# Performance work log

Hardware: AMD Instinct MI355X
Metric: run time of the kernel (lower is better)

The kernel has to match this reference:

```python
import jax, jax.numpy as jnp
import numpy as np

N, E = 8192, 16384
IN_C, HID = 64, 64
ALPHA, BETA = -1.5, -0.5
DENSITY = 0.004


def setup_inputs() -> dict:
    key = jax.random.key(0)
    k_x, k_b, k_w0, k_w1 = jax.random.split(key, 4)
    x_0 = jax.random.normal(k_x, (N, IN_C), dtype=jnp.float32)
    # sparse binary incidence matrix (stored dense, as in the original module)
    B1 = (jax.random.uniform(k_b, (N, E)) < DENSITY).astype(jnp.float32)
    # guarantee every node and every hyperedge has at least one incidence
    B1 = B1.at[jnp.arange(N), jnp.arange(N) % E].set(1.0)
    B1 = B1.at[jnp.arange(E) % N, jnp.arange(E)].set(1.0)
    W0 = jax.random.normal(k_w0, (IN_C, HID), dtype=jnp.float32) * (1.0 / np.sqrt(IN_C))
    W1 = jax.random.normal(k_w1, (HID, HID), dtype=jnp.float32) * (1.0 / np.sqrt(HID))
    bias_0_to_1 = jnp.zeros((1, HID), dtype=jnp.float32)
    bias_1_to_0 = jnp.zeros((1, HID), dtype=jnp.float32)
    return {"x_0": x_0, "incidence_1": B1, "W0": W0, "W1": W1,
            "bias_0_to_1": bias_0_to_1, "bias_1_to_0": bias_1_to_0}


def _normalize_incidence(B1):
    # vectorized equivalent of the O(N*E) python double loop
    mask = (B1 != 0).astype(B1.dtype)                  # [N,E]
    edge_sum = B1.sum(axis=0)                          # [E] hyperedge sizes
    node_sum = B1.sum(axis=1)                          # [N] node degrees
    edge_norm = edge_sum ** ALPHA                      # [E]
    node_norm = node_sum ** BETA                       # [N]
    # edge_factor[i] = 1 / sum_j mask[i,j]*edge_norm[j]  (row mat-vec)
    row_fac = 1.0 / (mask @ edge_norm)                 # [N]
    # node_factor[j] = 1 / sum_i mask[i,j]*node_norm[i]  (col mat-vec)
    col_fac = 1.0 / (mask.T @ node_norm)               # [E]
    return B1 * (row_fac * node_norm)[:, None] * (edge_norm * col_fac)[None, :]


def reference(x_0, incidence_1, W0, W1, bias_0_to_1, bias_1_to_0):
    B = _normalize_incidence(incidence_1)              # [N,E]
    # conv 0 -> 1: x_1 = B^T @ (x_0 @ W0) + b
    x_1 = B.T @ (x_0 @ W0) + bias_0_to_1               # [E,HID]
    # conv 1 -> 0: x_0' = B @ (x_1 @ W1) + b
    x_0_out = B @ (x_1 @ W1) + bias_1_to_0             # [N,HID]
    return jax.nn.relu(x_0_out), jax.nn.relu(x_1)
```

## Files before the change

kernel.cpp:

```cpp
#include <hip/hip_runtime.h>
#include <hip/hip_bf16.h>
#include <stdint.h>

#define NN 8192
#define NE 16384
#define HIDW 64
#define RCAP 128
#define CCAP 96

#define OFF_ROWCNT   0u
#define OFF_COLCNT   (OFF_ROWCNT + NN*4u)
#define MEMSET_BYTES (OFF_COLCNT + NE*4u)
#define OFF_ENORM    MEMSET_BYTES
#define OFF_NNORM    (OFF_ENORM + NE*4u)
#define OFF_RSCALE   (OFF_NNORM + NN*4u)
#define OFF_CSCALE   (OFF_RSCALE + NN*4u)
#define OFF_CSR      (OFF_CSCALE + NE*4u)
#define OFF_CSC      (OFF_CSR + NN*RCAP*4u)
#define OFF_Y0       (OFF_CSC + (size_t)NE*CCAP*4u)
#define OFF_X1PRE    (OFF_Y0 + NN*HIDW*4u)
#define OFF_Z1       (OFF_X1PRE + (size_t)NE*HIDW*4u)

__global__ __launch_bounds__(256) void k_scan(const float* __restrict__ B1,
        uint32_t* __restrict__ row_cnt, uint32_t* __restrict__ col_cnt,
        uint32_t* __restrict__ csr_col, uint32_t* __restrict__ csc_row) {
    __shared__ uint32_t rcur;
    const int tid = threadIdx.x;
    const int i = blockIdx.x;
    if (tid == 0) rcur = 0;
    __syncthreads();
    const long long base = (long long)i * NE;
    const int phase = i & 15;
    for (int it0 = 0; it0 < 16; ++it0) {
        int it = (it0 + phase) & 15;
        int local = it * 1024 + tid * 4;
        float4 v = *reinterpret_cast<const float4*>(B1 + base + local);
        float vs[4] = {v.x, v.y, v.z, v.w};
        #pragma unroll
        for (int q = 0; q < 4; ++q) {
            if (vs[q] != 0.0f) {
                uint32_t j = (uint32_t)(local + q);
                uint32_t p = atomicAdd(&rcur, 1u);
                if (p < RCAP) csr_col[(uint32_t)i * RCAP + p] = j;
                uint32_t qq = atomicAdd(&col_cnt[j], 1u);
                if (qq < CCAP) csc_row[j * CCAP + qq] = (uint32_t)i;
            }
        }
    }
    __syncthreads();
    if (tid == 0) row_cnt[i] = (rcur < RCAP) ? rcur : RCAP;
}

__global__ void k_norms(const uint32_t* __restrict__ row_cnt,
                        const uint32_t* __restrict__ col_cnt,
                        float* __restrict__ node_norm, float* __restrict__ edge_norm) {
    int idx = blockIdx.x * blockDim.x + threadIdx.x;
    if (idx < NE) { float s = (float)col_cnt[idx]; edge_norm[idx] = 1.0f / (s * sqrtf(s)); }
    if (idx < NN) { float s = (float)row_cnt[idx]; node_norm[idx] = 1.0f / sqrtf(s); }
}

__global__ __launch_bounds__(256) void k_scales(
        const uint32_t* __restrict__ row_cnt, const uint32_t* __restrict__ col_cnt,
        const uint32_t* __restrict__ csr_col, const uint32_t* __restrict__ csc_row,
        const float* __restrict__ node_norm, const float* __restrict__ edge_norm,
        float* __restrict__ rowscale, float* __restrict__ colscale) {
    int w = blockIdx.x * 4 + (threadIdx.x >> 6);
    int lane = threadIdx.x & 63;
    float s = 0.f;
    if (w < NN) {
        uint32_t c = row_cnt[w];
        const uint32_t* p = csr_col + (uint32_t)w * RCAP;
        for (uint32_t t = lane; t < c; t += 64) s += edge_norm[p[t]];
        #pragma unroll
        for (int off = 32; off >= 1; off >>= 1) s += __shfl_xor(s, off);
        if (lane == 0) rowscale[w] = node_norm[w] / s;
    } else {
        int j = w - NN;
        uint32_t c = col_cnt[j]; if (c > CCAP) c = CCAP;
        const uint32_t* p = csc_row + (uint32_t)j * CCAP;
        for (uint32_t t = lane; t < c; t += 64) s += node_norm[p[t]];
        #pragma unroll
        for (int off = 32; off >= 1; off >>= 1) s += __shfl_xor(s, off);
        if (lane == 0) colscale[j] = edge_norm[j] / s;
    }
}

__global__ __launch_bounds__(256) void k_gemm64(const float* __restrict__ X,
        const float* __restrict__ W, const float* __restrict__ scale,
        float* __restrict__ Y) {
    __shared__ float ws[64 * 64];
    __shared__ float xs[4][64];
    int tid = threadIdx.x;
    int c = tid & 63, rr = tid >> 6;
    for (int k = tid; k < 4096; k += 256) ws[k] = W[k];
    int row0 = blockIdx.x * 4;
    xs[rr][c] = X[(row0 + rr) * 64 + c];
    __syncthreads();
    float acc = 0.f;
    #pragma unroll
    for (int k = 0; k < 64; ++k) acc = fmaf(xs[rr][k], ws[k * 64 + c], acc);
    Y[(row0 + rr) * 64 + c] = scale[row0 + rr] * acc;
}

__global__ __launch_bounds__(256) void k_edge_gather(
        const uint32_t* __restrict__ col_cnt, const uint32_t* __restrict__ csc_row,
        const float* __restrict__ colscale, const float* __restrict__ y0s,
        const float* __restrict__ bias01, float* __restrict__ x1pre,
        float* __restrict__ out1) {
    int w = threadIdx.x >> 6, lane = threadIdx.x & 63;
    int j = blockIdx.x * 4 + w;
    uint32_t e = col_cnt[j]; if (e > CCAP) e = CCAP;
    const uint32_t* p = csc_row + (uint32_t)j * CCAP;
    float acc = 0.f;
    for (uint32_t t = 0; t < e; ++t) {
        uint32_t i = p[t];
        acc += y0s[i * 64 + lane];
    }
    float val = colscale[j] * acc + bias01[lane];
    x1pre[j * 64 + lane] = val;
    out1[j * 64 + lane] = fmaxf(val, 0.f);
}

__global__ __launch_bounds__(256) void k_node_gather(
        const uint32_t* __restrict__ row_cnt, const uint32_t* __restrict__ csr_col,
        const float* __restrict__ rowscale, const float* __restrict__ z1s,
        const float* __restrict__ bias10, float* __restrict__ out0) {
    int w = threadIdx.x >> 6, lane = threadIdx.x & 63;
    int i = blockIdx.x * 4 + w;
    uint32_t e = row_cnt[i];
    const uint32_t* p = csr_col + (uint32_t)i * RCAP;
    float acc = 0.f;
    for (uint32_t t = 0; t < e; ++t) {
        uint32_t j = p[t];
        acc += z1s[j * 64 + lane];
    }
    out0[i * 64 + lane] = fmaxf(rowscale[i] * acc + bias10[lane], 0.f);
}

extern "C" void kernel_launch(void* const* d_in, const int* in_sizes, int n_in,
                              void* d_out, int out_size, void* d_ws, size_t ws_size,
                              hipStream_t stream) {
    const float* x0  = (const float*)d_in[0];
    const float* B1  = (const float*)d_in[1];
    const float* W0  = (const float*)d_in[2];
    const float* W1  = (const float*)d_in[3];
    const float* b01 = (const float*)d_in[4];
    const float* b10 = (const float*)d_in[5];
    float* out = (float*)d_out;
    char* ws = (char*)d_ws;

    uint32_t* row_cnt = (uint32_t*)(ws + OFF_ROWCNT);
    uint32_t* col_cnt = (uint32_t*)(ws + OFF_COLCNT);
    float*    enorm   = (float*)(ws + OFF_ENORM);
    float*    nnorm   = (float*)(ws + OFF_NNORM);
    float*    rscale  = (float*)(ws + OFF_RSCALE);
    float*    cscale  = (float*)(ws + OFF_CSCALE);
    uint32_t* csr_col = (uint32_t*)(ws + OFF_CSR);
    uint32_t* csc_row = (uint32_t*)(ws + OFF_CSC);
    float*    y0      = (float*)(ws + OFF_Y0);
    float*    x1pre   = (float*)(ws + OFF_X1PRE);
    float*    z1      = (float*)(ws + OFF_Z1);

    hipMemsetAsync(d_ws, 0, MEMSET_BYTES, stream);

    k_scan<<<NN, 256, 0, stream>>>(B1, row_cnt, col_cnt, csr_col, csc_row);
    k_norms<<<NE / 256, 256, 0, stream>>>(row_cnt, col_cnt, nnorm, enorm);
    k_scales<<<(NN + NE) / 4, 256, 0, stream>>>(row_cnt, col_cnt, csr_col, csc_row,
            nnorm, enorm, rscale, cscale);
    k_gemm64<<<NN / 4, 256, 0, stream>>>(x0, W0, rscale, y0);
    k_edge_gather<<<NE / 4, 256, 0, stream>>>(col_cnt, csc_row, cscale, y0,
            b01, x1pre, out + NN * HIDW);
    k_gemm64<<<NE / 4, 256, 0, stream>>>(x1pre, W1, cscale, z1);
    k_node_gather<<<NN / 4, 256, 0, stream>>>(row_cnt, csr_col, rscale, z1, b10, out);
}
```

Before: 816.9 us.

## Fuse norm computation into scales kernel and vectorize gathers with float4

Result: faster. 766.9 us (-6.1%).

```diff
diff --git a/kernel.cpp b/kernel.cpp
--- a/kernel.cpp
+++ b/kernel.cpp
@@ -4,22 +4,19 @@
 
 #define NN 8192
 #define NE 16384
-#define HIDW 64
 #define RCAP 128
 #define CCAP 96
 
-#define OFF_ROWCNT   0u
-#define OFF_COLCNT   (OFF_ROWCNT + NN*4u)
-#define MEMSET_BYTES (OFF_COLCNT + NE*4u)
-#define OFF_ENORM    MEMSET_BYTES
-#define OFF_NNORM    (OFF_ENORM + NE*4u)
-#define OFF_RSCALE   (OFF_NNORM + NN*4u)
+#define OFF_COLCNT   0u
+#define MEMSET_BYTES (NE*4u)
+#define OFF_ROWCNT   MEMSET_BYTES
+#define OFF_RSCALE   (OFF_ROWCNT + NN*4u)
 #define OFF_CSCALE   (OFF_RSCALE + NN*4u)
 #define OFF_CSR      (OFF_CSCALE + NE*4u)
 #define OFF_CSC      (OFF_CSR + NN*RCAP*4u)
-#define OFF_Y0       (OFF_CSC + (size_t)NE*CCAP*4u)
-#define OFF_X1PRE    (OFF_Y0 + NN*HIDW*4u)
-#define OFF_Z1       (OFF_X1PRE + (size_t)NE*HIDW*4u)
+#define OFF_Y0       (OFF_CSC + NE*CCAP*4u)
+#define OFF_X1PRE    (OFF_Y0 + NN*64*4u)
+#define OFF_Z1       (OFF_X1PRE + NE*64*4u)
 
 __global__ __launch_bounds__(256) void k_scan(const float* __restrict__ B1,
         uint32_t* __restrict__ row_cnt, uint32_t* __restrict__ col_cnt,
@@ -30,9 +27,7 @@
     if (tid == 0) rcur = 0;
     __syncthreads();
     const long long base = (long long)i * NE;
-    const int phase = i & 15;
-    for (int it0 = 0; it0 < 16; ++it0) {
-        int it = (it0 + phase) & 15;
+    for (int it = 0; it < 16; ++it) {
         int local = it * 1024 + tid * 4;
         float4 v = *reinterpret_cast<const float4*>(B1 + base + local);
         float vs[4] = {v.x, v.y, v.z, v.w};
@@ -51,18 +46,9 @@
     if (tid == 0) row_cnt[i] = (rcur < RCAP) ? rcur : RCAP;
 }
 
-__global__ void k_norms(const uint32_t* __restrict__ row_cnt,
-                        const uint32_t* __restrict__ col_cnt,
-                        float* __restrict__ node_norm, float* __restrict__ edge_norm) {
-    int idx = blockIdx.x * blockDim.x + threadIdx.x;
-    if (idx < NE) { float s = (float)col_cnt[idx]; edge_norm[idx] = 1.0f / (s * sqrtf(s)); }
-    if (idx < NN) { float s = (float)row_cnt[idx]; node_norm[idx] = 1.0f / sqrtf(s); }
-}
-
 __global__ __launch_bounds__(256) void k_scales(
         const uint32_t* __restrict__ row_cnt, const uint32_t* __restrict__ col_cnt,
         const uint32_t* __restrict__ csr_col, const uint32_t* __restrict__ csc_row,
-        const float* __restrict__ node_norm, const float* __restrict__ edge_norm,
         float* __restrict__ rowscale, float* __restrict__ colscale) {
     int w = blockIdx.x * 4 + (threadIdx.x >> 6);
     int lane = threadIdx.x & 63;
@@ -70,18 +56,26 @@
     if (w < NN) {
         uint32_t c = row_cnt[w];
         const uint32_t* p = csr_col + (uint32_t)w * RCAP;
-        for (uint32_t t = lane; t < c; t += 64) s += edge_norm[p[t]];
+        for (uint32_t t = lane; t < c; t += 64) {
+            float cj = (float)col_cnt[p[t]];
+            s += 1.0f / (cj * sqrtf(cj));
+        }
         #pragma unroll
         for (int off = 32; off >= 1; off >>= 1) s += __shfl_xor(s, off);
-        if (lane == 0) rowscale[w] = node_norm[w] / s;
+        if (lane == 0) rowscale[w] = 1.0f / (sqrtf((float)c) * s);
     } else {
         int j = w - NN;
-        uint32_t c = col_cnt[j]; if (c > CCAP) c = CCAP;
+        uint32_t c = col_cnt[j];
+        uint32_t cl = c > CCAP ? CCAP : c;
         const uint32_t* p = csc_row + (uint32_t)j * CCAP;
-        for (uint32_t t = lane; t < c; t += 64) s += node_norm[p[t]];
+        for (uint32_t t = lane; t < cl; t += 64) {
+            float ri = (float)row_cnt[p[t]];
+            s += 1.0f / sqrtf(ri);
+        }
         #pragma unroll
         for (int off = 32; off >= 1; off >>= 1) s += __shfl_xor(s, off);
-        if (lane == 0) colscale[j] = edge_norm[j] / s;
+        float cf = (float)c;
+        if (lane == 0) colscale[j] = 1.0f / (cf * sqrtf(cf) * s);
     }
 }
 
@@ -111,14 +105,27 @@
     int j = blockIdx.x * 4 + w;
     uint32_t e = col_cnt[j]; if (e > CCAP) e = CCAP;
     const uint32_t* p = csc_row + (uint32_t)j * CCAP;
-    float acc = 0.f;
-    for (uint32_t t = 0; t < e; ++t) {
+    int g = lane >> 4, fl = lane & 15;
+    float4 acc = make_float4(0.f, 0.f, 0.f, 0.f);
+    for (uint32_t t = g; t < e; t += 4) {
         uint32_t i = p[t];
-        acc += y0s[i * 64 + lane];
+        const float4 v = *reinterpret_cast<const float4*>(y0s + i * 64u + fl * 4);
+        acc.x += v.x; acc.y += v.y; acc.z += v.z; acc.w += v.w;
     }
-    float val = colscale[j] * acc + bias01[lane];
-    x1pre[j * 64 + lane] = val;
-    out1[j * 64 + lane] = fmaxf(val, 0.f);
+    acc.x += __shfl_xor(acc.x, 16); acc.y += __shfl_xor(acc.y, 16);
+    acc.z += __shfl_xor(acc.z, 16); acc.w += __shfl_xor(acc.w, 16);
+    acc.x += __shfl_xor(acc.x, 32); acc.y += __shfl_xor(acc.y, 32);
+    acc.z += __shfl_xor(acc.z, 32); acc.w += __shfl_xor(acc.w, 32);
+    if (g == 0) {
+        float cs = colscale[j];
+        const float4 bb = *reinterpret_cast<const float4*>(bias01 + fl * 4);
+        float4 val = make_float4(fmaf(cs, acc.x, bb.x), fmaf(cs, acc.y, bb.y),
+                                 fmaf(cs, acc.z, bb.z), fmaf(cs, acc.w, bb.w));
+        *reinterpret_cast<float4*>(x1pre + j * 64u + fl * 4) = val;
+        float4 r = make_float4(fmaxf(val.x, 0.f), fmaxf(val.y, 0.f),
+                               fmaxf(val.z, 0.f), fmaxf(val.w, 0.f));
+        *reinterpret_cast<float4*>(out1 + j * 64u + fl * 4) = r;
+    }
 }
 
 __global__ __launch_bounds__(256) void k_node_gather(
@@ -129,12 +136,26 @@
     int i = blockIdx.x * 4 + w;
     uint32_t e = row_cnt[i];
     const uint32_t* p = csr_col + (uint32_t)i * RCAP;
-    float acc = 0.f;
-    for (uint32_t t = 0; t < e; ++t) {
-        uint32_t j = p[t];
-        acc += z1s[j * 64 + lane];
+    int g = lane >> 4, fl = lane & 15;
+    float4 acc = make_float4(0.f, 0.f, 0.f, 0.f);
+    for (uint32_t t = g; t < e; t += 4) {
+        uint32_t jj = p[t];
+        const float4 v = *reinterpret_cast<const float4*>(z1s + jj * 64u + fl * 4);
+        acc.x += v.x; acc.y += v.y; acc.z += v.z; acc.w += v.w;
     }
-    out0[i * 64 + lane] = fmaxf(rowscale[i] * acc + bias10[lane], 0.f);
+    acc.x += __shfl_xor(acc.x, 16); acc.y += __shfl_xor(acc.y, 16);
+    acc.z += __shfl_xor(acc.z, 16); acc.w += __shfl_xor(acc.w, 16);
+    acc.x += __shfl_xor(acc.x, 32); acc.y += __shfl_xor(acc.y, 32);
+    acc.z += __shfl_xor(acc.z, 32); acc.w += __shfl_xor(acc.w, 32);
+    if (g == 0) {
+        float rs = rowscale[i];
+        const float4 bb = *reinterpret_cast<const float4*>(bias10 + fl * 4);
+        float4 val = make_float4(fmaf(rs, acc.x, bb.x), fmaf(rs, acc.y, bb.y),
+                                 fmaf(rs, acc.z, bb.z), fmaf(rs, acc.w, bb.w));
+        float4 r = make_float4(fmaxf(val.x, 0.f), fmaxf(val.y, 0.f),
+                               fmaxf(val.z, 0.f), fmaxf(val.w, 0.f));
+        *reinterpret_cast<float4*>(out0 + i * 64u + fl * 4) = r;
+    }
 }
 
 extern "C" void kernel_launch(void* const* d_in, const int* in_sizes, int n_in,
@@ -149,10 +170,8 @@
     float* out = (float*)d_out;
     char* ws = (char*)d_ws;
 
+    uint32_t* col_cnt = (uint32_t*)(ws + OFF_COLCNT);
     uint32_t* row_cnt = (uint32_t*)(ws + OFF_ROWCNT);
-    uint32_t* col_cnt = (uint32_t*)(ws + OFF_COLCNT);
-    float*    enorm   = (float*)(ws + OFF_ENORM);
-    float*    nnorm   = (float*)(ws + OFF_NNORM);
     float*    rscale  = (float*)(ws + OFF_RSCALE);
     float*    cscale  = (float*)(ws + OFF_CSCALE);
     uint32_t* csr_col = (uint32_t*)(ws + OFF_CSR);
@@ -161,15 +180,14 @@
     float*    x1pre   = (float*)(ws + OFF_X1PRE);
     float*    z1      = (float*)(ws + OFF_Z1);
 
-    hipMemsetAsync(d_ws, 0, MEMSET_BYTES, stream);
+    hipMemsetAsync(col_cnt, 0, MEMSET_BYTES, stream);
 
     k_scan<<<NN, 256, 0, stream>>>(B1, row_cnt, col_cnt, csr_col, csc_row);
-    k_norms<<<NE / 256, 256, 0, stream>>>(row_cnt, col_cnt, nnorm, enorm);
     k_scales<<<(NN + NE) / 4, 256, 0, stream>>>(row_cnt, col_cnt, csr_col, csc_row,
-            nnorm, enorm, rscale, cscale);
+            rscale, cscale);
     k_gemm64<<<NN / 4, 256, 0, stream>>>(x0, W0, rscale, y0);
     k_edge_gather<<<NE / 4, 256, 0, stream>>>(col_cnt, csc_row, cscale, y0,
-            b01, x1pre, out + NN * HIDW);
+            b01, x1pre, out + NN * 64);
     k_gemm64<<<NE / 4, 256, 0, stream>>>(x1pre, W1, cscale, z1);
     k_node_gather<<<NN / 4, 256, 0, stream>>>(row_cnt, csr_col, rscale, z1, b10, out);
 }
```
